# Optimization experiments

Measured on AMD Instinct MI355X. Metric: run time of the kernel, lower is better.

## Reference

```python
import jax, jax.numpy as jnp
import numpy as np
import itertools

KH = KW = 3
N_NZ = 5
K_OUT = 126  # C(9,5) -> all patterns, matches capped n_kernels
C_IN = 128


def setup_inputs() -> dict:
    key = jax.random.key(0)
    k1, k2 = jax.random.split(key)
    inputs = jax.random.normal(k1, (32, 112, 112, C_IN), dtype=jnp.float32)
    # sparse_kernel: (n_non_zero, in_channels, kernels), glorot-ish scale
    scale = (2.0 / (N_NZ * C_IN + K_OUT)) ** 0.5
    sparse_kernel = jax.random.normal(k2, (N_NZ, C_IN, K_OUT), dtype=jnp.float32) * scale
    bias = jnp.zeros((K_OUT,), dtype=jnp.float32)
    # deterministic unique sparsity patterns: all C(9,5) flat-position combos
    patterns = jnp.asarray(
        np.array(list(itertools.combinations(range(KH * KW), N_NZ)), dtype=np.int32)
    )  # (K_OUT, N_NZ) flat positions in [0, 9)
    return {"inputs": inputs, "sparse_kernel": sparse_kernel, "bias": bias, "patterns": patterns}


def reference(inputs, sparse_kernel, bias, patterns):
    k_out = patterns.shape[0]
    c_in = sparse_kernel.shape[1]
    kk = jnp.arange(k_out)[:, None]  # (K,1) broadcasts against (K,N)
    # scatter: dense_flat[pos, :, k] = sparse_kernel[n, :, k]
    updates = jnp.transpose(sparse_kernel, (2, 0, 1))  # (K, N, Cin)
    dense_flat = jnp.zeros((KH * KW, c_in, k_out), dtype=inputs.dtype)
    dense_flat = dense_flat.at[patterns, :, kk].set(updates)
    dense_kernel = dense_flat.reshape(KH, KW, c_in, k_out)
    out = jax.lax.conv_general_dilated(
        inputs, dense_kernel, window_strides=(1, 1), padding="SAME",
        dimension_numbers=("NHWC", "HWIO", "NHWC"))
    return jax.nn.relu(out + bias)
```

## Files before the change

kernel.cpp:

```cpp
#include <hip/hip_runtime.h>
#include <hip/hip_bf16.h>


typedef __attribute__((ext_vector_type(8))) __bf16 bf16x8;
typedef __attribute__((ext_vector_type(4))) float f32x4;

__device__ __forceinline__ unsigned short f2bf(float f) {
  unsigned int u = __builtin_bit_cast(unsigned int, f);
  u += 0x7fffu + ((u >> 16) & 1u);
  return (unsigned short)(u >> 16);
}

__global__ __launch_bounds__(256) void build_B(const float* __restrict__ sk,
                                               const int* __restrict__ patterns,
                                               unsigned short* __restrict__ Bws) {
  int idx = blockIdx.x * 256 + threadIdx.x;
  if (idx >= 9 * 128 * 128) return;
  int c = idx & 127;
  int n = (idx >> 7) & 127;
  int p = idx >> 14;
  float v = 0.f;
  if (n < 126) {
#pragma unroll
    for (int j = 0; j < 5; ++j)
      if (patterns[n * 5 + j] == p) v = sk[(j * 128 + c) * 126 + n];
  }
  int cc = c >> 5, cl = c & 31;
  Bws[(((p * 4 + cc) * 128) + n) * 32 + cl] = f2bf(v);
}

__global__ __launch_bounds__(256) void conv_main(const float* __restrict__ in,
                                                 const unsigned short* __restrict__ Bws,
                                                 const float* __restrict__ bias,
                                                 float* __restrict__ out) {
  __shared__ unsigned short Alds[3 * 114 * 40];
  __shared__ unsigned short Blds[2][128 * 40];

  const int tid = threadIdx.x;
  const int bid = blockIdx.x;
  const int nimg = bid / 112;
  const int y = bid - nimg * 112;
  const int lane = tid & 63;
  const int w = tid >> 6;
  const int quad = lane >> 4;
  const int lrow = lane & 15;

  const float* inb = in + (size_t)nimg * 112 * 112 * 128;

  f32x4 acc[7][2];
#pragma unroll
  for (int mt = 0; mt < 7; ++mt) { acc[mt][0] = (f32x4)0.f; acc[mt][1] = (f32x4)0.f; }

  auto stageA = [&](int cc) {
#pragma unroll
    for (int it = 0; it < 11; ++it) {
      int i = tid + it * 256;
      if (i < 2736) {
        int c4 = i & 7;
        int rest = i >> 3;
        int r = rest / 114;
        int hx = rest - r * 114;
        int gy = y + r - 1;
        int gx = hx - 1;
        float4 v = make_float4(0.f, 0.f, 0.f, 0.f);
        if ((unsigned)gy < 112u && (unsigned)gx < 112u)
          v = *(const float4*)(inb + ((size_t)gy * 112 + gx) * 128 + cc * 32 + c4 * 4);
        ushort4 s;
        s.x = f2bf(v.x); s.y = f2bf(v.y); s.z = f2bf(v.z); s.w = f2bf(v.w);
        *(ushort4*)&Alds[(r * 114 + hx) * 40 + c4 * 4] = s;
      }
    }
  };

  const int i0 = tid, i1 = tid + 256;
  const int d0 = (i0 >> 2) * 40 + (i0 & 3) * 8;
  const int d1 = (i1 >> 2) * 40 + (i1 & 3) * 8;
  auto bsrc = [&](int t, int i) -> const uint4* {
    int cc = t / 9, p = t - cc * 9;
    int n = i >> 2, q = i & 3;
    return (const uint4*)(Bws + (((p * 4 + cc) * 128 + n) * 32 + q * 8));
  };

  stageA(0);
  {
    uint4 pb0 = *bsrc(0, i0), pb1 = *bsrc(0, i1);
    *(uint4*)&Blds[0][d0] = pb0;
    *(uint4*)&Blds[0][d1] = pb1;
  }
  __syncthreads();

#pragma unroll 1
  for (int t = 0; t < 36; ++t) {
    const int cc = t / 9;
    const int p = t - cc * 9;
    const int buf = t & 1;
    const bool pre = (t < 35);
    uint4 nb0, nb1;
    if (pre) { nb0 = *bsrc(t + 1, i0); nb1 = *bsrc(t + 1, i1); }

    const int r = p / 3;
    const int px = p - r * 3;
    const int abase = (r * 114 + px + lrow) * 40 + quad * 8;

    bf16x8 bf0 = *(const bf16x8*)&Blds[buf][(w * 32 + lrow) * 40 + quad * 8];
    bf16x8 bf1 = *(const bf16x8*)&Blds[buf][(w * 32 + 16 + lrow) * 40 + quad * 8];
#pragma unroll
    for (int mt = 0; mt < 7; ++mt) {
      bf16x8 a = *(const bf16x8*)&Alds[abase + mt * 16 * 40];
      acc[mt][0] = __builtin_amdgcn_mfma_f32_16x16x32_bf16(a, bf0, acc[mt][0], 0, 0, 0);
      acc[mt][1] = __builtin_amdgcn_mfma_f32_16x16x32_bf16(a, bf1, acc[mt][1], 0, 0, 0);
    }

    if (pre) {
      *(uint4*)&Blds[buf ^ 1][d0] = nb0;
      *(uint4*)&Blds[buf ^ 1][d1] = nb1;
    }
    __syncthreads();
    if (p == 8 && cc < 3) { stageA(cc + 1); __syncthreads(); }
  }

  const int k0 = w * 32 + lrow;
  const int k1 = k0 + 16;
  const float bv0 = bias[k0 < 126 ? k0 : 125];
  const float bv1 = bias[k1 < 126 ? k1 : 125];
  float* outrow = out + ((size_t)(nimg * 112 + y)) * 112 * 126;
#pragma unroll
  for (int mt = 0; mt < 7; ++mt) {
#pragma unroll
    for (int rg = 0; rg < 4; ++rg) {
      int x = mt * 16 + quad * 4 + rg;
      float* o = outrow + (size_t)x * 126;
      if (k0 < 126) { float v = acc[mt][0][rg] + bv0; o[k0] = v > 0.f ? v : 0.f; }
      if (k1 < 126) { float v = acc[mt][1][rg] + bv1; o[k1] = v > 0.f ? v : 0.f; }
    }
  }
}

extern "C" void kernel_launch(void* const* d_in, const int* in_sizes, int n_in,
                              void* d_out, int out_size, void* d_ws, size_t ws_size,
                              hipStream_t stream) {
  const float* in = (const float*)d_in[0];
  const float* sk = (const float*)d_in[1];
  const float* bias = (const float*)d_in[2];
  const int* patterns = (const int*)d_in[3];
  float* out = (float*)d_out;
  unsigned short* Bws = (unsigned short*)d_ws;

  build_B<<<dim3(576), dim3(256), 0, stream>>>(sk, patterns, Bws);
  conv_main<<<dim3(32 * 112), dim3(256), 0, stream>>>(in, Bws, bias, out);
}
```

Measured before the change: 525.1 us.

## Prefetch next A chunk into registers and load B fragments directly from global

Removes the B shared-memory double buffer. Each wave now loads its B fragments for all 9 taps straight from global memory into registers, once per channel chunk. The next input chunk is loaded into registers before the 63 MFMAs run and written to LDS afterwards, which hides global latency and cuts the barriers per block from 36+ to about 8. It also asks for 2 blocks per CU through launch bounds, so register pressure rises (44 float4 prefetch registers, 18 bf16x8 B registers and 56 accumulators) and may cause spills.

```diff
diff --git a/kernel.cpp b/kernel.cpp
--- a/kernel.cpp
+++ b/kernel.cpp
@@ -29,12 +29,11 @@
   Bws[(((p * 4 + cc) * 128) + n) * 32 + cl] = f2bf(v);
 }
 
-__global__ __launch_bounds__(256) void conv_main(const float* __restrict__ in,
-                                                 const unsigned short* __restrict__ Bws,
-                                                 const float* __restrict__ bias,
-                                                 float* __restrict__ out) {
+__global__ __launch_bounds__(256, 2) void conv_main(const float* __restrict__ in,
+                                                    const unsigned short* __restrict__ Bws,
+                                                    const float* __restrict__ bias,
+                                                    float* __restrict__ out) {
   __shared__ unsigned short Alds[3 * 114 * 40];
-  __shared__ unsigned short Blds[2][128 * 40];
 
   const int tid = threadIdx.x;
   const int bid = blockIdx.x;
@@ -51,7 +50,26 @@
 #pragma unroll
   for (int mt = 0; mt < 7; ++mt) { acc[mt][0] = (f32x4)0.f; acc[mt][1] = (f32x4)0.f; }
 
-  auto stageA = [&](int cc) {
+  float4 pf[11];
+  auto loadA = [&](int cc) {
+#pragma unroll
+    for (int it = 0; it < 11; ++it) {
+      int i = tid + it * 256;
+      float4 v = make_float4(0.f, 0.f, 0.f, 0.f);
+      if (i < 2736) {
+        int c4 = i & 7;
+        int rest = i >> 3;
+        int r = rest / 114;
+        int hx = rest - r * 114;
+        int gy = y + r - 1;
+        int gx = hx - 1;
+        if ((unsigned)gy < 112u && (unsigned)gx < 112u)
+          v = *(const float4*)(inb + ((size_t)gy * 112 + gx) * 128 + cc * 32 + c4 * 4);
+      }
+      pf[it] = v;
+    }
+  };
+  auto writeA = [&]() {
 #pragma unroll
     for (int it = 0; it < 11; ++it) {
       int i = tid + it * 256;
@@ -60,63 +78,48 @@
         int rest = i >> 3;
         int r = rest / 114;
         int hx = rest - r * 114;
-        int gy = y + r - 1;
-        int gx = hx - 1;
-        float4 v = make_float4(0.f, 0.f, 0.f, 0.f);
-        if ((unsigned)gy < 112u && (unsigned)gx < 112u)
-          v = *(const float4*)(inb + ((size_t)gy * 112 + gx) * 128 + cc * 32 + c4 * 4);
         ushort4 s;
-        s.x = f2bf(v.x); s.y = f2bf(v.y); s.z = f2bf(v.z); s.w = f2bf(v.w);
+        s.x = f2bf(pf[it].x); s.y = f2bf(pf[it].y);
+        s.z = f2bf(pf[it].z); s.w = f2bf(pf[it].w);
         *(ushort4*)&Alds[(r * 114 + hx) * 40 + c4 * 4] = s;
       }
     }
   };
 
-  const int i0 = tid, i1 = tid + 256;
-  const int d0 = (i0 >> 2) * 40 + (i0 & 3) * 8;
-  const int d1 = (i1 >> 2) * 40 + (i1 & 3) * 8;
-  auto bsrc = [&](int t, int i) -> const uint4* {
-    int cc = t / 9, p = t - cc * 9;
-    int n = i >> 2, q = i & 3;
-    return (const uint4*)(Bws + (((p * 4 + cc) * 128 + n) * 32 + q * 8));
-  };
-
-  stageA(0);
-  {
-    uint4 pb0 = *bsrc(0, i0), pb1 = *bsrc(0, i1);
-    *(uint4*)&Blds[0][d0] = pb0;
-    *(uint4*)&Blds[0][d1] = pb1;
-  }
+  loadA(0);
+  writeA();
   __syncthreads();
 
 #pragma unroll 1
-  for (int t = 0; t < 36; ++t) {
-    const int cc = t / 9;
-    const int p = t - cc * 9;
-    const int buf = t & 1;
-    const bool pre = (t < 35);
-    uint4 nb0, nb1;
-    if (pre) { nb0 = *bsrc(t + 1, i0); nb1 = *bsrc(t + 1, i1); }
+  for (int cc = 0; cc < 4; ++cc) {
+    bf16x8 b[9][2];
+#pragma unroll
+    for (int p = 0; p < 9; ++p)
+#pragma unroll
+      for (int j = 0; j < 2; ++j)
+        b[p][j] = *(const bf16x8*)(Bws +
+            (((size_t)(p * 4 + cc) * 128 + w * 32 + j * 16 + lrow) * 32 + quad * 8));
 
-    const int r = p / 3;
-    const int px = p - r * 3;
-    const int abase = (r * 114 + px + lrow) * 40 + quad * 8;
+    if (cc < 3) loadA(cc + 1);
 
-    bf16x8 bf0 = *(const bf16x8*)&Blds[buf][(w * 32 + lrow) * 40 + quad * 8];
-    bf16x8 bf1 = *(const bf16x8*)&Blds[buf][(w * 32 + 16 + lrow) * 40 + quad * 8];
 #pragma unroll
-    for (int mt = 0; mt < 7; ++mt) {
-      bf16x8 a = *(const bf16x8*)&Alds[abase + mt * 16 * 40];
-      acc[mt][0] = __builtin_amdgcn_mfma_f32_16x16x32_bf16(a, bf0, acc[mt][0], 0, 0, 0);
-      acc[mt][1] = __builtin_amdgcn_mfma_f32_16x16x32_bf16(a, bf1, acc[mt][1], 0, 0, 0);
+    for (int p = 0; p < 9; ++p) {
+      const int r = p / 3;
+      const int px = p - r * 3;
+      const int abase = (r * 114 + px + lrow) * 40 + quad * 8;
+#pragma unroll
+      for (int mt = 0; mt < 7; ++mt) {
+        bf16x8 a = *(const bf16x8*)&Alds[abase + mt * 16 * 40];
+        acc[mt][0] = __builtin_amdgcn_mfma_f32_16x16x32_bf16(a, b[p][0], acc[mt][0], 0, 0, 0);
+        acc[mt][1] = __builtin_amdgcn_mfma_f32_16x16x32_bf16(a, b[p][1], acc[mt][1], 0, 0, 0);
+      }
     }
 
-    if (pre) {
-      *(uint4*)&Blds[buf ^ 1][d0] = nb0;
-      *(uint4*)&Blds[buf ^ 1][d1] = nb1;
+    if (cc < 3) {
+      __syncthreads();
+      writeA();
+      __syncthreads();
     }
-    __syncthreads();
-    if (p == 8 && cc < 3) { stageA(cc + 1); __syncthreads(); }
   }
 
   const int k0 = w * 32 + lrow;
```

Measured after the change: 434.0 us. 1.21x faster.
